# Kernel optimization log

Hardware: AMD Instinct MI355X
Metric: run time of the kernel (lower is better)

## Reference

```python
import jax, jax.numpy as jnp
import numpy as np
import math

EMBED_DIM = 1024
NUM_HEADS = 16
HEAD_DIM = EMBED_DIM // NUM_HEADS  # 64
BLOCK = 64
SPARSITY = 0.05
BATCH = 2
SEQ = 2048


def _block_pattern(seq_len, block_size, sparsity_ratio, is_causal):
    """Faithful replication of _create_hilbert_aware_block_pattern (use_hilbert_pattern=True)."""
    nb = seq_len // block_size
    total = nb * nb
    keep = int(total * (1.0 - sparsity_ratio))
    idx = [(i, i) for i in range(nb)]
    band = max(1, int(math.sqrt(keep - nb) / 2))
    for i in range(nb):
        for o in range(1, band + 1):
            if i + o < nb:
                idx.append((i, i + o))
                if not is_causal:
                    idx.append((i + o, i))
            if (not is_causal) and i - o >= 0:
                idx.append((i, i - o))
    for skip in (2, 4, 8, 16):
        if len(idx) >= keep:
            break
        for i in range(0, nb - skip, skip):
            if len(idx) < keep:
                idx.append((i, i + skip))
                if (not is_causal) and len(idx) < keep:
                    idx.append((i + skip, i))
    uniq = sorted(set(idx))  # set-dedup as in original; sorted for determinism (no truncation occurs at these sizes)
    if is_causal:
        uniq = [(r, c) for r, c in uniq if r >= c]
    uniq = uniq[:keep]
    rows = np.array([r for r, c in uniq], dtype=np.int32)
    cols = np.array([c for r, c in uniq], dtype=np.int32)
    return rows, cols


ROWS, COLS = _block_pattern(SEQ, BLOCK, SPARSITY, is_causal=False)  # P = 752 blocks


def setup_inputs() -> dict:
    rng = jax.random.key(0)
    ks = jax.random.split(rng, 7)
    wscale = EMBED_DIM ** -0.5  # keep pre-softmax logits in a sane range
    return {
        "query": jax.random.normal(ks[0], (BATCH, SEQ, EMBED_DIM), jnp.float32),
        "key": jax.random.normal(ks[1], (BATCH, SEQ, EMBED_DIM), jnp.float32),
        "value": jax.random.normal(ks[2], (BATCH, SEQ, EMBED_DIM), jnp.float32),
        "Wq": jax.random.normal(ks[3], (EMBED_DIM, EMBED_DIM), jnp.float32) * wscale,
        "Wk": jax.random.normal(ks[4], (EMBED_DIM, EMBED_DIM), jnp.float32) * wscale,
        "Wv": jax.random.normal(ks[5], (EMBED_DIM, EMBED_DIM), jnp.float32) * wscale,
        "Wo": jax.random.normal(ks[6], (EMBED_DIM, EMBED_DIM), jnp.float32) * wscale,
    }


def reference(query, key, value, Wq, Wk, Wv, Wo):
    B, S, E = query.shape
    nb = S // BLOCK
    scale = HEAD_DIM ** -0.5

    def proj_blocks(x, W):
        # [B,S,E] -> [B,H,nb,block,hd]
        h = (x @ W.T).reshape(B, S, NUM_HEADS, HEAD_DIM).transpose(0, 2, 1, 3)
        return h.reshape(B, NUM_HEADS, nb, BLOCK, HEAD_DIM)

    qb = proj_blocks(query, Wq)
    kb = proj_blocks(key, Wk)
    vb = proj_blocks(value, Wv)

    rows = jnp.asarray(ROWS)
    cols = jnp.asarray(COLS)
    qg = qb[:, :, rows]  # [B,H,P,block,hd]
    kg = kb[:, :, cols]
    vg = vb[:, :, cols]

    # Per-block softmax (NOT online softmax across column blocks) exactly as the torch loop
    scores = jnp.einsum('bhpqd,bhpkd->bhpqk', qg, kg) * scale  # [B,H,P,block,block]
    attn = jax.nn.softmax(scores, axis=-1)
    ob = jnp.einsum('bhpqk,bhpkd->bhpqd', attn, vg)  # [B,H,P,block,hd]

    # Accumulate (sum) contributions into each query row block, as the torch += loop does
    acc = jax.ops.segment_sum(ob.transpose(2, 0, 1, 3, 4), rows, num_segments=nb)  # [nb,B,H,block,hd]
    out = acc.transpose(1, 2, 0, 3, 4).reshape(B, NUM_HEADS, S, HEAD_DIM)
    out = out.transpose(0, 2, 1, 3).reshape(B, S, E)
    return out @ Wo.T
```

## Files before the change

kernel.cpp:

```cpp
#include <hip/hip_runtime.h>
#include <hip/hip_bf16.h>

typedef __attribute__((ext_vector_type(4))) float f32x4;
typedef __attribute__((ext_vector_type(8))) short bfx8;

#define K_DIM 1024
#define N_DIM 1024

__device__ __forceinline__ ushort f2bf(float f) {
    uint u = __float_as_uint(f);
    u += 0x7fffu + ((u >> 16) & 1u);
    return (ushort)(u >> 16);
}

__device__ __forceinline__ void gll16(const ushort* g, ushort* l) {
    __builtin_amdgcn_global_load_lds(
        (const __attribute__((address_space(1))) uint*)g,
        (__attribute__((address_space(3))) uint*)l,
        16, 0, 0);
}

__global__ __launch_bounds__(256) void cvt_all(
    const float* __restrict__ q, const float* __restrict__ k, const float* __restrict__ v,
    const float* __restrict__ wq, const float* __restrict__ wk,
    const float* __restrict__ wv, const float* __restrict__ wo,
    ushort* __restrict__ ws)
{
    const int IN4 = 1 << 20;
    const int W4  = 1 << 18;
    const int total = 3*IN4 + 4*W4;
    ushort4* dst4 = reinterpret_cast<ushort4*>(ws);
    for (int u = blockIdx.x*blockDim.x + threadIdx.x; u < total; u += gridDim.x*blockDim.x) {
        const float* src; int local, off;
        if (u < 3*IN4) {
            int op = u >> 20;
            local = u & (IN4-1);
            src = op==0 ? q : (op==1 ? k : v);
            off = op * IN4;
        } else {
            int t = u - 3*IN4;
            int op = t >> 18;
            local = t & (W4-1);
            src = op==0 ? wq : (op==1 ? wk : (op==2 ? wv : wo));
            off = 3*IN4 + op*W4;
        }
        float4 f = reinterpret_cast<const float4*>(src)[local];
        ushort4 o;
        o.x = f2bf(f.x); o.y = f2bf(f.y); o.z = f2bf(f.z); o.w = f2bf(f.w);
        dst4[off + local] = o;
    }
}

template<int MODE>
__device__ __forceinline__ void gemm_body(
    const ushort* __restrict__ A, const ushort* __restrict__ Bw,
    ushort* __restrict__ C, float* __restrict__ Cf,
    int blk, ushort* As, ushort* Bs)
{
    const int tid  = threadIdx.x;
    const int lane = tid & 63;
    const int wave = tid >> 6;
    const int tn = blk & 7;
    const int tm = blk >> 3;
    const int wr = wave >> 1, wc = wave & 1;

    int goff[4];
    #pragma unroll
    for (int t = 0; t < 4; ++t) {
        int u = wave*256 + t*64 + lane;
        int row = u >> 3;
        int col = (u & 7) ^ (row & 7);
        goff[t] = row * K_DIM + col * 8;
    }
    const ushort* Abase = A  + (size_t)tm * 128 * K_DIM;
    const ushort* Bbase = Bw + (size_t)tn * 128 * K_DIM;

    f32x4 acc[4][4];
    #pragma unroll
    for (int a = 0; a < 4; ++a)
        #pragma unroll
        for (int b2 = 0; b2 < 4; ++b2)
            acc[a][b2] = (f32x4){0.f, 0.f, 0.f, 0.f};

    for (int k0 = 0; k0 < K_DIM; k0 += 64) {
        __syncthreads();
        #pragma unroll
        for (int t = 0; t < 4; ++t) {
            gll16(Abase + k0 + goff[t], As + (wave*256 + t*64)*8);
            gll16(Bbase + k0 + goff[t], Bs + (wave*256 + t*64)*8);
        }
        __syncthreads();
        #pragma unroll
        for (int kk = 0; kk < 2; ++kk) {
            bfx8 af[4], bfr[4];
            #pragma unroll
            for (int mi = 0; mi < 4; ++mi) {
                int row  = wr*64 + mi*16 + (lane & 15);
                int unit = kk*4 + (lane >> 4);
                af[mi] = *reinterpret_cast<const bfx8*>(&As[row*64 + (unit ^ (row & 7))*8]);
            }
            #pragma unroll
            for (int ni = 0; ni < 4; ++ni) {
                int row  = wc*64 + ni*16 + (lane & 15);
                int unit = kk*4 + (lane >> 4);
                bfr[ni] = *reinterpret_cast<const bfx8*>(&Bs[row*64 + (unit ^ (row & 7))*8]);
            }
            #pragma unroll
            for (int mi = 0; mi < 4; ++mi)
                #pragma unroll
                for (int ni = 0; ni < 4; ++ni)
                    acc[mi][ni] = __builtin_amdgcn_mfma_f32_16x16x32_bf16(af[mi], bfr[ni], acc[mi][ni], 0, 0, 0);
        }
    }
    #pragma unroll
    for (int mi = 0; mi < 4; ++mi)
      #pragma unroll
      for (int ni = 0; ni < 4; ++ni)
        #pragma unroll
        for (int i = 0; i < 4; ++i) {
            int gr = tm*128 + wr*64 + mi*16 + (lane >> 4)*4 + i;
            int gc = tn*128 + wc*64 + ni*16 + (lane & 15);
            if constexpr (MODE == 0) {
                int b = gr >> 11, s = gr & 2047, h = gc >> 6, d = gc & 63;
                C[(((size_t)(b*16 + h))*2048 + s)*64 + d] = f2bf(acc[mi][ni][i]);
            } else if constexpr (MODE == 1) {
                int b = gr >> 11, s = gr & 2047, h = gc >> 6, d = gc & 63;
                C[(((size_t)(b*16 + h))*64 + d)*2048 + s] = f2bf(acc[mi][ni][i]);
            } else {
                Cf[(size_t)gr*N_DIM + gc] = acc[mi][ni][i];
            }
        }
}

__global__ __launch_bounds__(256) void proj_kernel(
    const ushort* __restrict__ qb, const ushort* __restrict__ kb, const ushort* __restrict__ vb,
    const ushort* __restrict__ wqb, const ushort* __restrict__ wkb, const ushort* __restrict__ wvb,
    ushort* __restrict__ Qp, ushort* __restrict__ Kp, ushort* __restrict__ Vt)
{
    __shared__ ushort As[128*64];
    __shared__ ushort Bs[128*64];
    int op = blockIdx.y;
    if (op == 0)      gemm_body<0>(qb, wqb, Qp, nullptr, blockIdx.x, As, Bs);
    else if (op == 1) gemm_body<0>(kb, wkb, Kp, nullptr, blockIdx.x, As, Bs);
    else              gemm_body<1>(vb, wvb, Vt, nullptr, blockIdx.x, As, Bs);
}

__global__ __launch_bounds__(256) void outproj_kernel(
    const ushort* __restrict__ AO, const ushort* __restrict__ wob, float* __restrict__ out)
{
    __shared__ ushort As[128*64];
    __shared__ ushort Bs[128*64];
    gemm_body<2>(AO, wob, nullptr, out, blockIdx.x, As, Bs);
}

__global__ __launch_bounds__(256) void attn_kernel(
    const ushort* __restrict__ Qp, const ushort* __restrict__ Kp,
    const ushort* __restrict__ Vt, ushort* __restrict__ AO)
{
    const int blk = blockIdx.x;
    const int r = blk & 31;
    const int h = (blk >> 5) & 15;
    const int b = blk >> 9;
    const int tid  = threadIdx.x;
    const int lane = tid & 63;
    const int wave = tid >> 6;

    __shared__ ushort Ks[2][4096];
    __shared__ ushort Vs[2][4096];
    __shared__ ushort QPs[4096];

    const ushort* Qb = Qp + (size_t)(b*16 + h) * 2048 * 64;
    const ushort* Kb = Kp + (size_t)(b*16 + h) * 2048 * 64;
    const ushort* Vb = Vt + (size_t)(b*16 + h) * 64 * 2048;

    int koff[2], voff[2];
    #pragma unroll
    for (int t = 0; t < 2; ++t) {
        int u = wave*128 + t*64 + lane;
        int row = u >> 3;
        int col = (u & 7) ^ (row & 7);
        koff[t] = row*64 + col*8;
        voff[t] = row*2048 + col*8;
    }

    int c0 = r - 15; if (c0 < 0) c0 = 0;
    int c1 = r + 15; if (c1 > 31) c1 = 31;

    #pragma unroll
    for (int t = 0; t < 2; ++t) {
        gll16(Qb + (size_t)r*4096 + koff[t], QPs + (wave*128 + t*64)*8);
        gll16(Kb + (size_t)c0*4096 + koff[t], &Ks[0][(wave*128 + t*64)*8]);
        gll16(Vb + (size_t)c0*64   + voff[t], &Vs[0][(wave*128 + t*64)*8]);
    }
    __syncthreads();

    bfx8 qf[2];
    #pragma unroll
    for (int kk = 0; kk < 2; ++kk) {
        int arow = wave*16 + (lane & 15);
        int unit = kk*4 + (lane >> 4);
        qf[kk] = *reinterpret_cast<const bfx8*>(&QPs[arow*64 + (unit ^ (arow & 7))*8]);
    }

    f32x4 acc_o[4];
    #pragma unroll
    for (int n = 0; n < 4; ++n) acc_o[n] = (f32x4){0.f,0.f,0.f,0.f};

    const float SC = 0.125f * 1.44269504f;
    int cur = 0;
    for (int c = c0; c <= c1; ++c) {
        if (c < c1) {
            #pragma unroll
            for (int t = 0; t < 2; ++t) {
                gll16(Kb + (size_t)(c+1)*4096 + koff[t], &Ks[cur^1][(wave*128 + t*64)*8]);
                gll16(Vb + (size_t)(c+1)*64   + voff[t], &Vs[cur^1][(wave*128 + t*64)*8]);
            }
        }

        f32x4 sc[4];
        #pragma unroll
        for (int n = 0; n < 4; ++n) sc[n] = (f32x4){0.f,0.f,0.f,0.f};
        #pragma unroll
        for (int kk = 0; kk < 2; ++kk) {
            #pragma unroll
            for (int n = 0; n < 4; ++n) {
                int brow = n*16 + (lane & 15);
                int unit = kk*4 + (lane >> 4);
                bfx8 kf = *reinterpret_cast<const bfx8*>(&Ks[cur][brow*64 + (unit ^ (brow & 7))*8]);
                sc[n] = __builtin_amdgcn_mfma_f32_16x16x32_bf16(qf[kk], kf, sc[n], 0,0,0);
            }
        }

        float pn[4][4]; float inv[4];
        #pragma unroll
        for (int i = 0; i < 4; ++i) {
            float ssum = 0.f;
            #pragma unroll
            for (int n = 0; n < 4; ++n) { float e = exp2f(sc[n][i]*SC); pn[n][i] = e; ssum += e; }
            #pragma unroll
            for (int msk = 1; msk <= 8; msk <<= 1) ssum += __shfl_xor(ssum, msk);
            inv[i] = __builtin_amdgcn_rcpf(ssum);
        }
        #pragma unroll
        for (int n = 0; n < 4; ++n)
            #pragma unroll
            for (int i = 0; i < 4; ++i) {
                int row  = wave*16 + (lane >> 4)*4 + i;
                int colv = n*16 + (lane & 15);
                QPs[row*64 + ((colv >> 3) ^ (row & 7))*8 + (colv & 7)] = f2bf(pn[n][i]*inv[i]);
            }

        #pragma unroll
        for (int kk = 0; kk < 2; ++kk) {
            int arow = wave*16 + (lane & 15);
            int unit = kk*4 + (lane >> 4);
            bfx8 pf = *reinterpret_cast<const bfx8*>(&QPs[arow*64 + (unit ^ (arow & 7))*8]);
            #pragma unroll
            for (int n = 0; n < 4; ++n) {
                int brow = n*16 + (lane & 15);
                bfx8 vf = *reinterpret_cast<const bfx8*>(&Vs[cur][brow*64 + (unit ^ (brow & 7))*8]);
                acc_o[n] = __builtin_amdgcn_mfma_f32_16x16x32_bf16(pf, vf, acc_o[n], 0,0,0);
            }
        }

        __syncthreads();
        cur ^= 1;
    }

    #pragma unroll
    for (int n = 0; n < 4; ++n)
        #pragma unroll
        for (int i = 0; i < 4; ++i) {
            int qrow = r*64 + wave*16 + (lane >> 4)*4 + i;
            int e    = h*64 + n*16 + (lane & 15);
            AO[((size_t)b*2048 + qrow)*1024 + e] = f2bf(acc_o[n][i]);
        }
}

extern "C" void kernel_launch(void* const* d_in, const int* in_sizes, int n_in,
                              void* d_out, int out_size, void* d_ws, size_t ws_size,
                              hipStream_t stream)
{
    (void)in_sizes; (void)n_in; (void)out_size; (void)ws_size;
    const float* q  = (const float*)d_in[0];
    const float* k  = (const float*)d_in[1];
    const float* v  = (const float*)d_in[2];
    const float* wq = (const float*)d_in[3];
    const float* wk = (const float*)d_in[4];
    const float* wv = (const float*)d_in[5];
    const float* wo = (const float*)d_in[6];

    ushort* ws = (ushort*)d_ws;
    const size_t IN_E = 4096ull * 1024ull;
    const size_t W_E  = 1024ull * 1024ull;
    ushort* qb  = ws;
    ushort* kb  = qb + IN_E;
    ushort* vb  = kb + IN_E;
    ushort* wqb = vb + IN_E;
    ushort* wkb = wqb + W_E;
    ushort* wvb = wkb + W_E;
    ushort* wob = wvb + W_E;
    ushort* Qp  = wob + W_E;
    ushort* Kp  = Qp + IN_E;
    ushort* Vt  = Kp + IN_E;
    ushort* AO  = Vt + IN_E;

    cvt_all<<<4096, 256, 0, stream>>>(q, k, v, wq, wk, wv, wo, ws);
    proj_kernel<<<dim3(256, 3), 256, 0, stream>>>(qb, kb, vb, wqb, wkb, wvb, Qp, Kp, Vt);
    attn_kernel<<<1024, 256, 0, stream>>>(Qp, Kp, Vt, AO);
    outproj_kernel<<<256, 256, 0, stream>>>(AO, wob, (float*)d_out);
}
```

Before: 259.5 us.

## Fuse input bf16 conversion into projection GEMM, share K/V tiles across row pairs

The fp32-to-bf16 conversion of the query, key and value activations moves into the projection GEMM's A-tile load, so only the weights still go through a separate conversion kernel. This removes a full write and re-read of the converted activations, but the A operand now arrives through register loads instead of direct-to-LDS loads. The attention kernel now uses 512 threads so each block handles two adjacent query row blocks and reuses each loaded K/V tile for both, with per-wave guards to keep each row's band exact. The softmax row-sum shuffles are replaced by DPP adds.

```diff
diff --git a/kernel.cpp b/kernel.cpp
--- a/kernel.cpp
+++ b/kernel.cpp
@@ -20,40 +20,35 @@
         16, 0, 0);
 }
 
-__global__ __launch_bounds__(256) void cvt_all(
-    const float* __restrict__ q, const float* __restrict__ k, const float* __restrict__ v,
+template<int CTRL>
+__device__ __forceinline__ float dpp_add(float x) {
+    int yi = __builtin_amdgcn_update_dpp(0, __float_as_int(x), CTRL, 0xf, 0xf, true);
+    return x + __int_as_float(yi);
+}
+
+__global__ __launch_bounds__(256) void cvt_w(
     const float* __restrict__ wq, const float* __restrict__ wk,
     const float* __restrict__ wv, const float* __restrict__ wo,
     ushort* __restrict__ ws)
 {
-    const int IN4 = 1 << 20;
-    const int W4  = 1 << 18;
-    const int total = 3*IN4 + 4*W4;
+    const int W4 = 1 << 18;
+    const int total = 4*W4;
     ushort4* dst4 = reinterpret_cast<ushort4*>(ws);
     for (int u = blockIdx.x*blockDim.x + threadIdx.x; u < total; u += gridDim.x*blockDim.x) {
-        const float* src; int local, off;
-        if (u < 3*IN4) {
-            int op = u >> 20;
-            local = u & (IN4-1);
-            src = op==0 ? q : (op==1 ? k : v);
-            off = op * IN4;
-        } else {
-            int t = u - 3*IN4;
-            int op = t >> 18;
-            local = t & (W4-1);
-            src = op==0 ? wq : (op==1 ? wk : (op==2 ? wv : wo));
-            off = 3*IN4 + op*W4;
-        }
+        int op = u >> 18;
+        int local = u & (W4-1);
+        const float* src = op==0 ? wq : (op==1 ? wk : (op==2 ? wv : wo));
         float4 f = reinterpret_cast<const float4*>(src)[local];
         ushort4 o;
         o.x = f2bf(f.x); o.y = f2bf(f.y); o.z = f2bf(f.z); o.w = f2bf(f.w);
-        dst4[off + local] = o;
+        dst4[u] = o;
     }
 }
 
 template<int MODE>
 __device__ __forceinline__ void gemm_body(
-    const ushort* __restrict__ A, const ushort* __restrict__ Bw,
+    const float* __restrict__ Af, const ushort* __restrict__ Ab,
+    const ushort* __restrict__ Bw,
     ushort* __restrict__ C, float* __restrict__ Cf,
     int blk, ushort* As, ushort* Bs)
 {
@@ -72,8 +67,9 @@
         int col = (u & 7) ^ (row & 7);
         goff[t] = row * K_DIM + col * 8;
     }
-    const ushort* Abase = A  + (size_t)tm * 128 * K_DIM;
-    const ushort* Bbase = Bw + (size_t)tn * 128 * K_DIM;
+    const ushort* Bbase  = Bw + (size_t)tn * 128 * K_DIM;
+    const float*  Afbase = (MODE < 2) ? Af + (size_t)tm * 128 * K_DIM : nullptr;
+    const ushort* Abbase = (MODE == 2) ? Ab + (size_t)tm * 128 * K_DIM : nullptr;
 
     f32x4 acc[4][4];
     #pragma unroll
@@ -85,9 +81,27 @@
     for (int k0 = 0; k0 < K_DIM; k0 += 64) {
         __syncthreads();
         #pragma unroll
-        for (int t = 0; t < 4; ++t) {
-            gll16(Abase + k0 + goff[t], As + (wave*256 + t*64)*8);
+        for (int t = 0; t < 4; ++t)
             gll16(Bbase + k0 + goff[t], Bs + (wave*256 + t*64)*8);
+        if constexpr (MODE == 2) {
+            #pragma unroll
+            for (int t = 0; t < 4; ++t)
+                gll16(Abbase + k0 + goff[t], As + (wave*256 + t*64)*8);
+        } else {
+            #pragma unroll
+            for (int t = 0; t < 4; ++t) {
+                int u = tid + t*256;
+                int row = u >> 3, col = u & 7;
+                const float* s = Afbase + (size_t)row*K_DIM + k0 + col*8;
+                float4 f0 = *reinterpret_cast<const float4*>(s);
+                float4 f1 = *reinterpret_cast<const float4*>(s + 4);
+                ushort4 lo, hi;
+                lo.x = f2bf(f0.x); lo.y = f2bf(f0.y); lo.z = f2bf(f0.z); lo.w = f2bf(f0.w);
+                hi.x = f2bf(f1.x); hi.y = f2bf(f1.y); hi.z = f2bf(f1.z); hi.w = f2bf(f1.w);
+                ushort* d = &As[row*64 + (col ^ (row & 7))*8];
+                *reinterpret_cast<ushort4*>(d)     = lo;
+                *reinterpret_cast<ushort4*>(d + 4) = hi;
+            }
         }
         __syncthreads();
         #pragma unroll
@@ -133,16 +147,16 @@
 }
 
 __global__ __launch_bounds__(256) void proj_kernel(
-    const ushort* __restrict__ qb, const ushort* __restrict__ kb, const ushort* __restrict__ vb,
+    const float* __restrict__ q, const float* __restrict__ k, const float* __restrict__ v,
     const ushort* __restrict__ wqb, const ushort* __restrict__ wkb, const ushort* __restrict__ wvb,
     ushort* __restrict__ Qp, ushort* __restrict__ Kp, ushort* __restrict__ Vt)
 {
     __shared__ ushort As[128*64];
     __shared__ ushort Bs[128*64];
     int op = blockIdx.y;
-    if (op == 0)      gemm_body<0>(qb, wqb, Qp, nullptr, blockIdx.x, As, Bs);
-    else if (op == 1) gemm_body<0>(kb, wkb, Kp, nullptr, blockIdx.x, As, Bs);
-    else              gemm_body<1>(vb, wvb, Vt, nullptr, blockIdx.x, As, Bs);
+    if (op == 0)      gemm_body<0>(q, nullptr, wqb, Qp, nullptr, blockIdx.x, As, Bs);
+    else if (op == 1) gemm_body<0>(k, nullptr, wkb, Kp, nullptr, blockIdx.x, As, Bs);
+    else              gemm_body<1>(v, nullptr, wvb, Vt, nullptr, blockIdx.x, As, Bs);
 }
 
 __global__ __launch_bounds__(256) void outproj_kernel(
@@ -150,48 +164,48 @@
 {
     __shared__ ushort As[128*64];
     __shared__ ushort Bs[128*64];
-    gemm_body<2>(AO, wob, nullptr, out, blockIdx.x, As, Bs);
-}
-
-__global__ __launch_bounds__(256) void attn_kernel(
+    gemm_body<2>(nullptr, AO, wob, nullptr, out, blockIdx.x, As, Bs);
+}
+
+__global__ __launch_bounds__(512) void attn_kernel(
     const ushort* __restrict__ Qp, const ushort* __restrict__ Kp,
     const ushort* __restrict__ Vt, ushort* __restrict__ AO)
 {
     const int blk = blockIdx.x;
-    const int r = blk & 31;
-    const int h = (blk >> 5) & 15;
-    const int b = blk >> 9;
+    const int g = blk & 15;
+    const int h = (blk >> 4) & 15;
+    const int b = blk >> 8;
+    const int r0 = g << 1;
     const int tid  = threadIdx.x;
     const int lane = tid & 63;
     const int wave = tid >> 6;
+    const int rw = r0 + (wave >> 2);
 
     __shared__ ushort Ks[2][4096];
     __shared__ ushort Vs[2][4096];
-    __shared__ ushort QPs[4096];
+    __shared__ ushort QPs[8192];
 
     const ushort* Qb = Qp + (size_t)(b*16 + h) * 2048 * 64;
     const ushort* Kb = Kp + (size_t)(b*16 + h) * 2048 * 64;
     const ushort* Vb = Vt + (size_t)(b*16 + h) * 64 * 2048;
 
-    int koff[2], voff[2];
+    const int krow = tid >> 3;
+    const int kcol = (tid & 7) ^ (krow & 7);
+    const int koff = krow*64   + kcol*8;
+    const int voff = krow*2048 + kcol*8;
+
+    int clo = r0 - 15; if (clo < 0) clo = 0;
+    int chi = r0 + 16; if (chi > 31) chi = 31;
+
     #pragma unroll
     for (int t = 0; t < 2; ++t) {
         int u = wave*128 + t*64 + lane;
         int row = u >> 3;
         int col = (u & 7) ^ (row & 7);
-        koff[t] = row*64 + col*8;
-        voff[t] = row*2048 + col*8;
-    }
-
-    int c0 = r - 15; if (c0 < 0) c0 = 0;
-    int c1 = r + 15; if (c1 > 31) c1 = 31;
-
-    #pragma unroll
-    for (int t = 0; t < 2; ++t) {
-        gll16(Qb + (size_t)r*4096 + koff[t], QPs + (wave*128 + t*64)*8);
-        gll16(Kb + (size_t)c0*4096 + koff[t], &Ks[0][(wave*128 + t*64)*8]);
-        gll16(Vb + (size_t)c0*64   + voff[t], &Vs[0][(wave*128 + t*64)*8]);
-    }
+        gll16(Qb + (size_t)(r0*64 + row)*64 + col*8, QPs + (wave*128 + t*64)*8);
+    }
+    gll16(Kb + (size_t)clo*4096 + koff, &Ks[0][wave*64*8]);
+    gll16(Vb + (size_t)clo*64   + voff, &Vs[0][wave*64*8]);
     __syncthreads();
 
     bfx8 qf[2];
@@ -208,58 +222,59 @@
 
     const float SC = 0.125f * 1.44269504f;
     int cur = 0;
-    for (int c = c0; c <= c1; ++c) {
-        if (c < c1) {
-            #pragma unroll
-            for (int t = 0; t < 2; ++t) {
-                gll16(Kb + (size_t)(c+1)*4096 + koff[t], &Ks[cur^1][(wave*128 + t*64)*8]);
-                gll16(Vb + (size_t)(c+1)*64   + voff[t], &Vs[cur^1][(wave*128 + t*64)*8]);
-            }
-        }
-
-        f32x4 sc[4];
-        #pragma unroll
-        for (int n = 0; n < 4; ++n) sc[n] = (f32x4){0.f,0.f,0.f,0.f};
-        #pragma unroll
-        for (int kk = 0; kk < 2; ++kk) {
-            #pragma unroll
-            for (int n = 0; n < 4; ++n) {
-                int brow = n*16 + (lane & 15);
+    for (int c = clo; c <= chi; ++c) {
+        if (c < chi) {
+            gll16(Kb + (size_t)(c+1)*4096 + koff, &Ks[cur^1][wave*64*8]);
+            gll16(Vb + (size_t)(c+1)*64   + voff, &Vs[cur^1][wave*64*8]);
+        }
+
+        if (c >= rw - 15 && c <= rw + 15) {
+            f32x4 sc[4];
+            #pragma unroll
+            for (int n = 0; n < 4; ++n) sc[n] = (f32x4){0.f,0.f,0.f,0.f};
+            #pragma unroll
+            for (int kk = 0; kk < 2; ++kk) {
+                #pragma unroll
+                for (int n = 0; n < 4; ++n) {
+                    int brow = n*16 + (lane & 15);
+                    int unit = kk*4 + (lane >> 4);
+                    bfx8 kf = *reinterpret_cast<const bfx8*>(&Ks[cur][brow*64 + (unit ^ (brow & 7))*8]);
+                    sc[n] = __builtin_amdgcn_mfma_f32_16x16x32_bf16(qf[kk], kf, sc[n], 0,0,0);
+                }
+            }
+
+            float pn[4][4]; float inv[4];
+            #pragma unroll
+            for (int i = 0; i < 4; ++i) {
+                float ssum = 0.f;
+                #pragma unroll
+                for (int n = 0; n < 4; ++n) { float e = exp2f(sc[n][i]*SC); pn[n][i] = e; ssum += e; }
+                ssum = dpp_add<0xB1>(ssum);
+                ssum = dpp_add<0x4E>(ssum);
+                ssum = dpp_add<0x124>(ssum);
+                ssum = dpp_add<0x128>(ssum);
+                inv[i] = __builtin_amdgcn_rcpf(ssum);
+            }
+            #pragma unroll
+            for (int n = 0; n < 4; ++n)
+                #pragma unroll
+                for (int i = 0; i < 4; ++i) {
+                    int row  = wave*16 + (lane >> 4)*4 + i;
+                    int colv = n*16 + (lane & 15);
+                    QPs[row*64 + ((colv >> 3) ^ (row & 7))*8 + (colv & 7)] = f2bf(pn[n][i]*inv[i]);
+                }
+
+            #pragma unroll
+            for (int kk = 0; kk < 2; ++kk) {
+                int arow = wave*16 + (lane & 15);
                 int unit = kk*4 + (lane >> 4);
-                bfx8 kf = *reinterpret_cast<const bfx8*>(&Ks[cur][brow*64 + (unit ^ (brow & 7))*8]);
-                sc[n] = __builtin_amdgcn_mfma_f32_16x16x32_bf16(qf[kk], kf, sc[n], 0,0,0);
-            }
-        }
-
-        float pn[4][4]; float inv[4];
-        #pragma unroll
-        for (int i = 0; i < 4; ++i) {
-            float ssum = 0.f;
-            #pragma unroll
-            for (int n = 0; n < 4; ++n) { float e = exp2f(sc[n][i]*SC); pn[n][i] = e; ssum += e; }
-            #pragma unroll
-            for (int msk = 1; msk <= 8; msk <<= 1) ssum += __shfl_xor(ssum, msk);
-            inv[i] = __builtin_amdgcn_rcpf(ssum);
-        }
-        #pragma unroll
-        for (int n = 0; n < 4; ++n)
-            #pragma unroll
-            for (int i = 0; i < 4; ++i) {
-                int row  = wave*16 + (lane >> 4)*4 + i;
-                int colv = n*16 + (lane & 15);
-                QPs[row*64 + ((colv >> 3) ^ (row & 7))*8 + (colv & 7)] = f2bf(pn[n][i]*inv[i]);
-            }
-
-        #pragma unroll
-        for (int kk = 0; kk < 2; ++kk) {
-            int arow = wave*16 + (lane & 15);
-            int unit = kk*4 + (lane >> 4);
-            bfx8 pf = *reinterpret_cast<const bfx8*>(&QPs[arow*64 + (unit ^ (arow & 7))*8]);
-            #pragma unroll
-            for (int n = 0; n < 4; ++n) {
-                int brow = n*16 + (lane & 15);
-                bfx8 vf = *reinterpret_cast<const bfx8*>(&Vs[cur][brow*64 + (unit ^ (brow & 7))*8]);
-                acc_o[n] = __builtin_amdgcn_mfma_f32_16x16x32_bf16(pf, vf, acc_o[n], 0,0,0);
+                bfx8 pf = *reinterpret_cast<const bfx8*>(&QPs[arow*64 + (unit ^ (arow & 7))*8]);
+                #pragma unroll
+                for (int n = 0; n < 4; ++n) {
+                    int brow = n*16 + (lane & 15);
+                    bfx8 vf = *reinterpret_cast<const bfx8*>(&Vs[cur][brow*64 + (unit ^ (brow & 7))*8]);
+                    acc_o[n] = __builtin_amdgcn_mfma_f32_16x16x32_bf16(pf, vf, acc_o[n], 0,0,0);
+                }
             }
         }
 
@@ -271,7 +286,7 @@
     for (int n = 0; n < 4; ++n)
         #pragma unroll
         for (int i = 0; i < 4; ++i) {
-            int qrow = r*64 + wave*16 + (lane >> 4)*4 + i;
+            int qrow = r0*64 + wave*16 + (lane >> 4)*4 + i;
             int e    = h*64 + n*16 + (lane & 15);
             AO[((size_t)b*2048 + qrow)*1024 + e] = f2bf(acc_o[n][i]);
         }
@@ -293,10 +308,7 @@
     ushort* ws = (ushort*)d_ws;
     const size_t IN_E = 4096ull * 1024ull;
     const size_t W_E  = 1024ull * 1024ull;
-    ushort* qb  = ws;
-    ushort* kb  = qb + IN_E;
-    ushort* vb  = kb + IN_E;
-    ushort* wqb = vb + IN_E;
+    ushort* wqb = ws;
     ushort* wkb = wqb + W_E;
     ushort* wvb = wkb + W_E;
     ushort* wob = wvb + W_E;
@@ -305,8 +317,8 @@
     ushort* Vt  = Kp + IN_E;
     ushort* AO  = Vt + IN_E;
 
-    cvt_all<<<4096, 256, 0, stream>>>(q, k, v, wq, wk, wv, wo, ws);
-    proj_kernel<<<dim3(256, 3), 256, 0, stream>>>(qb, kb, vb, wqb, wkb, wvb, Qp, Kp, Vt);
-    attn_kernel<<<1024, 256, 0, stream>>>(Qp, Kp, Vt, AO);
+    cvt_w<<<1024, 256, 0, stream>>>(wq, wk, wv, wo, ws);
+    proj_kernel<<<dim3(256, 3), 256, 0, stream>>>(q, k, v, wqb, wkb, wvb, Qp, Kp, Vt);
+    attn_kernel<<<512, 512, 0, stream>>>(Qp, Kp, Vt, AO);
     outproj_kernel<<<256, 256, 0, stream>>>(AO, wob, (float*)d_out);
 }
```

Result: no change. 264.6 us (+2.0%).
